# Performance work log

Hardware: AMD Instinct MI355X
Metric: run time of the kernel (lower is better)

Reference implementation:

```python
import jax, jax.numpy as jnp
import numpy as np

STU_N, EXER_N, K_N, EMB = 20000, 20000, 128, 128
BATCH = 4096

def _pos(w):
    # PosLinear weight transform: 2*relu(-w) + w  (== |w|)
    return 2.0 * jax.nn.relu(-w) + w

def setup_inputs() -> dict:
    key = jax.random.key(0)
    ks = jax.random.split(key, 12)
    xav = lambda k, shape: jax.random.normal(k, shape, jnp.float32) * np.sqrt(2.0 / sum(shape))
    return {
        "stu_id": jax.random.randint(ks[0], (BATCH,), 0, STU_N, jnp.int32),
        "exer_id": jax.random.randint(ks[1], (BATCH,), 0, EXER_N, jnp.int32),
        "kq": jax.random.uniform(ks[2], (BATCH, K_N), jnp.float32),
        "student_q": xav(ks[3], (STU_N, EMB)),
        "exercise_k": xav(ks[4], (EXER_N, EMB)),
        "student_v": xav(ks[5], (STU_N, EMB)),
        "exercise_v": xav(ks[6], (EXER_N, EMB)),
        "knowledge_v": xav(ks[7], (K_N, EMB)),
        "W1": xav(ks[8], (EMB, 2 * EMB)), "b1": jnp.zeros((EMB,), jnp.float32),
        "W2": xav(ks[9], (EMB, 2 * EMB)), "b2": jnp.zeros((EMB,), jnp.float32),
        "W3": xav(ks[10], (1, EMB)), "b3": jnp.zeros((1,), jnp.float32),
    }

def reference(stu_id, exer_id, kq, student_q, exercise_k, student_v, exercise_v,
              knowledge_v, W1, b1, W2, b2, W3, b3):
    stu_q = student_q[stu_id]          # (B, D)
    exer_k = exercise_k[exer_id]       # (B, D)
    stu_v = student_v[stu_id]          # (B, D)
    exer_v = exercise_v[exer_id]       # (B, D)
    B, D = stu_v.shape
    K = knowledge_v.shape[0]

    kn = jnp.broadcast_to(knowledge_v[None, :, :], (B, K, D))
    stu_b = jnp.broadcast_to(stu_v[:, None, :], (B, K, D))
    exer_b = jnp.broadcast_to(exer_v[:, None, :], (B, K, D))

    # PosLinear 1/2 on concat([x, kn]) -> split GEMM avoids materializing concat
    W1p, W2p, W3p = _pos(W1), _pos(W2), _pos(W3)
    pref = jax.nn.sigmoid(jnp.einsum('bkd,ed->bke', jnp.concatenate([stu_b, kn], -1), W1p) + b1)
    diff = jax.nn.sigmoid(jnp.einsum('bkd,ed->bke', jnp.concatenate([exer_b, kn], -1), W2p) + b2)

    disc = jax.nn.sigmoid(stu_q * exer_k)              # (B, D)
    input_x = (pref - diff) * disc[:, None, :]         # (B, K, D)
    o = jax.nn.sigmoid(jnp.einsum('bkd,od->bko', input_x, W3p) + b3)  # (B, K, 1)

    sum_out = jnp.sum(o * kq[:, :, None], axis=1)      # (B, 1)
    count = jnp.sum(kq, axis=1, keepdims=True)         # (B, 1)
    return jnp.squeeze(sum_out / count)                # (B,)
```

## Files before the change

### kernel.cpp

```cpp
#include <hip/hip_runtime.h>

#define D  128
#define KN 128
#define NB 16
#define LOG2E 1.44269504088896340736f

typedef float f32x4  __attribute__((ext_vector_type(4)));
typedef float f32x16 __attribute__((ext_vector_type(16)));
typedef short s16x8  __attribute__((ext_vector_type(8)));

__device__ __forceinline__ float negexp(float v) {
    return __builtin_amdgcn_exp2f(v * -LOG2E);
}
__device__ __forceinline__ float sigf(float x) {
    return __builtin_amdgcn_rcpf(1.0f + negexp(x));
}
__device__ __forceinline__ unsigned short f2bf(float f) {
    unsigned u = __float_as_uint(f);
    return (unsigned short)((u + 0x7fffu + ((u >> 16) & 1u)) >> 16);
}
__device__ __forceinline__ s16x8 pack8(float4 a, float4 b) {
    s16x8 r;
    r[0]=(short)f2bf(a.x); r[1]=(short)f2bf(a.y); r[2]=(short)f2bf(a.z); r[3]=(short)f2bf(a.w);
    r[4]=(short)f2bf(b.x); r[5]=(short)f2bf(b.y); r[6]=(short)f2bf(b.z); r[7]=(short)f2bf(b.w);
    return r;
}
__device__ __forceinline__ s16x8 pack8abs(float4 a, float4 b) {
    s16x8 r;
    r[0]=(short)f2bf(fabsf(a.x)); r[1]=(short)f2bf(fabsf(a.y)); r[2]=(short)f2bf(fabsf(a.z)); r[3]=(short)f2bf(fabsf(a.w));
    r[4]=(short)f2bf(fabsf(b.x)); r[5]=(short)f2bf(fabsf(b.y)); r[6]=(short)f2bf(fabsf(b.z)); r[7]=(short)f2bf(fabsf(b.w));
    return r;
}

#define CORE(EA1, EA2, T, PZ, A0, A1) do {                                   \
    float x0_ = fmaf((EA1), (T).x, 1.0f);                                    \
    float x1_ = fmaf((EA1), (T).y, 1.0f);                                    \
    float y0_ = fmaf((EA2), (T).z, 1.0f);                                    \
    float y1_ = fmaf((EA2), (T).w, 1.0f);                                    \
    (A0) = fmaf((y0_ - x0_) * (PZ), __builtin_amdgcn_rcpf(x0_ * y0_), (A0)); \
    (A1) = fmaf((y1_ - x1_) * (PZ), __builtin_amdgcn_rcpf(x1_ * y1_), (A1)); \
} while (0)

#define TTILE(T, ACC) {                                                       \
    const int idx_ = (wid << 2) + (T);                                        \
    const char* Wsb_ = (idx_ < 16) ? W1s_base : W2s_base;                     \
    const int et_ = (idx_ >> 2) & 3, kt_ = idx_ & 3;                          \
    const int er_ = et_ * 32 + l31, kr_ = kt_ * 32 + l31;                     \
    const int eswz_ = (er_ & 7) << 4, kswz_ = (kr_ & 7) << 4;                 \
    _Pragma("unroll")                                                         \
    for (int q = 0; q < 8; ++q) {                                             \
        int dby = q * 32 + g32 * 16;                                          \
        s16x8 a_ = *(const s16x8*)(Wsb_ + er_ * 256 + (dby ^ eswz_));         \
        s16x8 b_ = *(const s16x8*)(KNs_base + kr_ * 256 + (dby ^ kswz_));     \
        ACC = __builtin_amdgcn_mfma_f32_32x32x16_bf16(a_, b_, ACC, 0, 0, 0);  \
    } }

#define TWRITE(T, ACC) {                                                      \
    const int idx_ = (wid << 2) + (T);                                        \
    const int et_ = (idx_ >> 2) & 3, kt_ = idx_ & 3;                          \
    const int slot_ = (idx_ < 16) ? 0 : 2;                                    \
    const float* bias_ = (idx_ < 16) ? b1 : b2;                               \
    const int k_ = kt_ * 32 + l31;                                            \
    const int kof_ = ((k_ >> 1) << 2) + (k_ & 1) + slot_;                     \
    _Pragma("unroll")                                                         \
    for (int r = 0; r < 16; ++r) {                                            \
        int e_ = et_ * 32 + (r & 3) + ((r >> 2) << 3) + (g32 << 2);           \
        TABf[e_ * 256 + kof_] = negexp(ACC[r] + bias_[e_]);                   \
    } }

__global__ __launch_bounds__(512, 1) void fused_kernel(
    const int* __restrict__ stu_id, const int* __restrict__ exer_id,
    const float* __restrict__ kq,
    const float* __restrict__ stu_q, const float* __restrict__ exer_k,
    const float* __restrict__ stu_v, const float* __restrict__ exer_v,
    const float* __restrict__ kn,
    const float* __restrict__ W1, const float* __restrict__ b1,
    const float* __restrict__ W2, const float* __restrict__ b2,
    const float* __restrict__ W3, const float* __restrict__ b3,
    float* __restrict__ out, int B)
{
    __shared__ float4 smem4[9728];
    __shared__ int sids[NB], eids[NB];

    float* TABf = (float*)smem4;
    float* EAf  = TABf + 32768;
    float* PZf  = EAf + 4096;
    char* KNs_base = (char*)smem4;
    char* W1s_base = KNs_base + 32768;
    char* W2s_base = KNs_base + 65536;

    const int tid  = threadIdx.x;
    const int b0   = blockIdx.x * NB;
    const int lane = tid & 63, wid = tid >> 6;
    const int l31 = lane & 31, g32 = lane >> 5;
    const int l15 = lane & 15, g16 = lane >> 4;

    if (tid < NB) {
        int b = b0 + tid;
        sids[tid] = stu_id[b < B ? b : 0];
        eids[tid] = exer_id[b < B ? b : 0];
    }
    for (int i = tid; i < 128 * 16; i += 512) {
        int row = i >> 4, c = i & 15;
        int byt = row * 256 + (((c << 4)) ^ ((row & 7) << 4));
        const float4* sk = (const float4*)(kn + (size_t)row * D + c * 8);
        *(s16x8*)(KNs_base + byt) = pack8(sk[0], sk[1]);
        const float4* s1 = (const float4*)(W1 + (size_t)row * (2 * D) + D + c * 8);
        *(s16x8*)(W1s_base + byt) = pack8abs(s1[0], s1[1]);
        const float4* s2 = (const float4*)(W2 + (size_t)row * (2 * D) + D + c * 8);
        *(s16x8*)(W2s_base + byt) = pack8abs(s2[0], s2[1]);
    }
    __syncthreads();

    f32x16 t0acc = {0}, t1acc = {0}, t2acc = {0}, t3acc = {0};
    TTILE(0, t0acc) TTILE(1, t1acc) TTILE(2, t2acc) TTILE(3, t3acc)

    const int sid_l = sids[l15], eid_l = eids[l15];
    const int erow  = wid * 16 + l15;
    f32x4 accS = {0, 0, 0, 0}, accE = {0, 0, 0, 0};
    #pragma unroll
    for (int q = 0; q < 4; ++q) {
        int d = q * 32 + g16 * 8;
        const float4* pa = (const float4*)(stu_v + (size_t)sid_l * D + d);
        const float4* pb = (const float4*)(W1 + (size_t)erow * (2 * D) + d);
        accS = __builtin_amdgcn_mfma_f32_16x16x32_bf16(
            pack8(pa[0], pa[1]), pack8abs(pb[0], pb[1]), accS, 0, 0, 0);
        const float4* pe = (const float4*)(exer_v + (size_t)eid_l * D + d);
        const float4* pc = (const float4*)(W2 + (size_t)erow * (2 * D) + d);
        accE = __builtin_amdgcn_mfma_f32_16x16x32_bf16(
            pack8(pe[0], pe[1]), pack8abs(pc[0], pc[1]), accE, 0, 0, 0);
    }
    #pragma unroll
    for (int r = 0; r < 4; ++r) {
        int b = g16 * 4 + r;
        int eo = b * 256 + 2 * erow;
        EAf[eo]     = negexp(accS[r]);
        EAf[eo + 1] = negexp(accE[r]);
    }
    {
        int b = tid >> 5, e4 = (tid & 31) << 2;
        float4 sq = *(const float4*)(stu_q + (size_t)sids[b] * D + e4);
        float4 ek = *(const float4*)(exer_k + (size_t)eids[b] * D + e4);
        float4 w3 = *(const float4*)(W3 + e4);
        float4 z;
        z.x = sigf(sq.x * ek.x) * fabsf(w3.x);
        z.y = sigf(sq.y * ek.y) * fabsf(w3.y);
        z.z = sigf(sq.z * ek.z) * fabsf(w3.z);
        z.w = sigf(sq.w * ek.w) * fabsf(w3.w);
        *(float4*)(PZf + b * D + e4) = z;
    }
    __syncthreads();

    TWRITE(0, t0acc) TWRITE(1, t1acc) TWRITE(2, t2acc) TWRITE(3, t3acc)
    __syncthreads();

    const float4* TAB4 = (const float4*)TABf;
    const float4* EA4  = (const float4*)EAf;
    const float2* PZ2  = (const float2*)PZf;
    const float b3v = b3[0];
    const int rA = 2 * wid, rB = 2 * wid + 1;
    const int bA = b0 + rA, bB = b0 + rB;

    float acc0a = 0.f, acc1a = 0.f, acc0b = 0.f, acc1b = 0.f;
    #pragma unroll 2
    for (int j = 0; j < D / 2; ++j) {
        float4 t0 = TAB4[(2 * j) * 64 + lane];
        float4 t1 = TAB4[(2 * j + 1) * 64 + lane];
        float4 eA = EA4[rA * 64 + j]; float2 zA = PZ2[rA * 64 + j];
        float4 eB = EA4[rB * 64 + j]; float2 zB = PZ2[rB * 64 + j];
        CORE(eA.x, eA.y, t0, zA.x, acc0a, acc1a);
        CORE(eA.z, eA.w, t1, zA.y, acc0a, acc1a);
        CORE(eB.x, eB.y, t0, zB.x, acc0b, acc1b);
        CORE(eB.z, eB.w, t1, zB.y, acc0b, acc1b);
    }

    float o0a = sigf(acc0a + b3v), o1a = sigf(acc1a + b3v);
    float o0b = sigf(acc0b + b3v), o1b = sigf(acc1b + b3v);
    float na = 0.f, da = 0.f, nb = 0.f, db = 0.f;
    if (bA < B) {
        float2 kqa = *(const float2*)(kq + (size_t)bA * D + 2 * lane);
        na = fmaf(o0a, kqa.x, o1a * kqa.y); da = kqa.x + kqa.y;
    }
    if (bB < B) {
        float2 kqb = *(const float2*)(kq + (size_t)bB * D + 2 * lane);
        nb = fmaf(o0b, kqb.x, o1b * kqb.y); db = kqb.x + kqb.y;
    }
    #pragma unroll
    for (int off = 32; off > 0; off >>= 1) {
        na += __shfl_xor(na, off); da += __shfl_xor(da, off);
        nb += __shfl_xor(nb, off); db += __shfl_xor(db, off);
    }
    if (lane == 0) {
        if (bA < B) out[bA] = na / da;
        if (bB < B) out[bB] = nb / db;
    }
}

extern "C" void kernel_launch(void* const* d_in, const int* in_sizes, int n_in,
                              void* d_out, int out_size, void* d_ws, size_t ws_size,
                              hipStream_t stream)
{
    const int*   stu_id      = (const int*)  d_in[0];
    const int*   exer_id     = (const int*)  d_in[1];
    const float* kq          = (const float*)d_in[2];
    const float* student_q   = (const float*)d_in[3];
    const float* exercise_k  = (const float*)d_in[4];
    const float* student_v   = (const float*)d_in[5];
    const float* exercise_v  = (const float*)d_in[6];
    const float* knowledge_v = (const float*)d_in[7];
    const float* W1 = (const float*)d_in[8];
    const float* b1 = (const float*)d_in[9];
    const float* W2 = (const float*)d_in[10];
    const float* b2 = (const float*)d_in[11];
    const float* W3 = (const float*)d_in[12];
    const float* b3 = (const float*)d_in[13];
    float* out = (float*)d_out;
    const int B = in_sizes[0];

    int nblk = (B + NB - 1) / NB;
    fused_kernel<<<nblk, 512, 0, stream>>>(
        stu_id, exer_id, kq, student_q, exercise_k, student_v, exercise_v,
        knowledge_v, W1, b1, W2, b2, W3, b3, out, B);
}
```

Before: 32.41 us.

## Split main loop over embedding dim across waves, reuse A fragments, reduce via LDS

The table GEMM now has each wave own one 32-row E tile of W1 or W2 and compute all four K tiles. This loads the A fragment once per step and reuses it across four MFMAs. The gathered stu_v/exer_v rows are prefetched into registers before the MFMA phase so global latency overlaps with it. The per-element core loop is re-partitioned so each wave handles 16 embedding columns for all 16 batch rows and reads each TAB row once instead of every wave reading all of them. Partial sums then go through an LDS reduction across waves, at the cost of an extra barrier pair, extra LDS traffic and more registers (16 float2 accumulators plus 16 float4 prefetch registers).

```diff
diff --git a/kernel.cpp b/kernel.cpp
--- a/kernel.cpp
+++ b/kernel.cpp
@@ -40,20 +40,6 @@
     (A0) = fmaf((y0_ - x0_) * (PZ), __builtin_amdgcn_rcpf(x0_ * y0_), (A0)); \
     (A1) = fmaf((y1_ - x1_) * (PZ), __builtin_amdgcn_rcpf(x1_ * y1_), (A1)); \
 } while (0)
-
-#define TTILE(T, ACC) {                                                       \
-    const int idx_ = (wid << 2) + (T);                                        \
-    const char* Wsb_ = (idx_ < 16) ? W1s_base : W2s_base;                     \
-    const int et_ = (idx_ >> 2) & 3, kt_ = idx_ & 3;                          \
-    const int er_ = et_ * 32 + l31, kr_ = kt_ * 32 + l31;                     \
-    const int eswz_ = (er_ & 7) << 4, kswz_ = (kr_ & 7) << 4;                 \
-    _Pragma("unroll")                                                         \
-    for (int q = 0; q < 8; ++q) {                                             \
-        int dby = q * 32 + g32 * 16;                                          \
-        s16x8 a_ = *(const s16x8*)(Wsb_ + er_ * 256 + (dby ^ eswz_));         \
-        s16x8 b_ = *(const s16x8*)(KNs_base + kr_ * 256 + (dby ^ kswz_));     \
-        ACC = __builtin_amdgcn_mfma_f32_32x32x16_bf16(a_, b_, ACC, 0, 0, 0);  \
-    } }
 
 #define TWRITE(T, ACC) {                                                      \
     const int idx_ = (wid << 2) + (T);                                        \
@@ -112,23 +98,49 @@
     }
     __syncthreads();
 
-    f32x16 t0acc = {0}, t1acc = {0}, t2acc = {0}, t3acc = {0};
-    TTILE(0, t0acc) TTILE(1, t1acc) TTILE(2, t2acc) TTILE(3, t3acc)
-
     const int sid_l = sids[l15], eid_l = eids[l15];
     const int erow  = wid * 16 + l15;
-    f32x4 accS = {0, 0, 0, 0}, accE = {0, 0, 0, 0};
+    float4 ga[8], ge[8];
     #pragma unroll
     for (int q = 0; q < 4; ++q) {
         int d = q * 32 + g16 * 8;
         const float4* pa = (const float4*)(stu_v + (size_t)sid_l * D + d);
+        ga[2*q] = pa[0]; ga[2*q+1] = pa[1];
+        const float4* pe = (const float4*)(exer_v + (size_t)eid_l * D + d);
+        ge[2*q] = pe[0]; ge[2*q+1] = pe[1];
+    }
+
+    f32x16 t0acc = {0}, t1acc = {0}, t2acc = {0}, t3acc = {0};
+    {
+        const char* Wsb = (wid < 4) ? W1s_base : W2s_base;
+        const int er = (wid & 3) * 32 + l31;
+        const int eswz = (er & 7) << 4;
+        const int kswz = (l31 & 7) << 4;
+        #pragma unroll
+        for (int q = 0; q < 8; ++q) {
+            int dby = q * 32 + g32 * 16;
+            s16x8 a_  = *(const s16x8*)(Wsb + er * 256 + (dby ^ eswz));
+            s16x8 bb0 = *(const s16x8*)(KNs_base + (  0 + l31) * 256 + (dby ^ kswz));
+            s16x8 bb1 = *(const s16x8*)(KNs_base + ( 32 + l31) * 256 + (dby ^ kswz));
+            s16x8 bb2 = *(const s16x8*)(KNs_base + ( 64 + l31) * 256 + (dby ^ kswz));
+            s16x8 bb3 = *(const s16x8*)(KNs_base + ( 96 + l31) * 256 + (dby ^ kswz));
+            t0acc = __builtin_amdgcn_mfma_f32_32x32x16_bf16(a_, bb0, t0acc, 0, 0, 0);
+            t1acc = __builtin_amdgcn_mfma_f32_32x32x16_bf16(a_, bb1, t1acc, 0, 0, 0);
+            t2acc = __builtin_amdgcn_mfma_f32_32x32x16_bf16(a_, bb2, t2acc, 0, 0, 0);
+            t3acc = __builtin_amdgcn_mfma_f32_32x32x16_bf16(a_, bb3, t3acc, 0, 0, 0);
+        }
+    }
+
+    f32x4 accS = {0, 0, 0, 0}, accE = {0, 0, 0, 0};
+    #pragma unroll
+    for (int q = 0; q < 4; ++q) {
+        int d = q * 32 + g16 * 8;
         const float4* pb = (const float4*)(W1 + (size_t)erow * (2 * D) + d);
         accS = __builtin_amdgcn_mfma_f32_16x16x32_bf16(
-            pack8(pa[0], pa[1]), pack8abs(pb[0], pb[1]), accS, 0, 0, 0);
-        const float4* pe = (const float4*)(exer_v + (size_t)eid_l * D + d);
+            pack8(ga[2*q], ga[2*q+1]), pack8abs(pb[0], pb[1]), accS, 0, 0, 0);
         const float4* pc = (const float4*)(W2 + (size_t)erow * (2 * D) + d);
         accE = __builtin_amdgcn_mfma_f32_16x16x32_bf16(
-            pack8(pe[0], pe[1]), pack8abs(pc[0], pc[1]), accE, 0, 0, 0);
+            pack8(ge[2*q], ge[2*q+1]), pack8abs(pc[0], pc[1]), accE, 0, 0, 0);
     }
     #pragma unroll
     for (int r = 0; r < 4; ++r) {
@@ -157,25 +169,47 @@
     const float4* TAB4 = (const float4*)TABf;
     const float4* EA4  = (const float4*)EAf;
     const float2* PZ2  = (const float2*)PZf;
+
+    float2 acc[16];
+    #pragma unroll
+    for (int r = 0; r < 16; ++r) acc[r] = make_float2(0.f, 0.f);
+
+    for (int jj = 0; jj < 8; ++jj) {
+        const int e0 = wid * 16 + 2 * jj;
+        const int jg = wid * 8 + jj;
+        float4 t0 = TAB4[e0 * 64 + lane];
+        float4 t1 = TAB4[(e0 + 1) * 64 + lane];
+        #pragma unroll
+        for (int r = 0; r < 16; ++r) {
+            float4 eA = EA4[r * 64 + jg];
+            float2 zA = PZ2[r * 64 + jg];
+            CORE(eA.x, eA.y, t0, zA.x, acc[r].x, acc[r].y);
+            CORE(eA.z, eA.w, t1, zA.y, acc[r].x, acc[r].y);
+        }
+    }
+    __syncthreads();
+
+    float2* RED = (float2*)TABf;
+    #pragma unroll
+    for (int r = 0; r < 16; ++r)
+        RED[(wid * 16 + r) * 64 + lane] = acc[r];
+    __syncthreads();
+
     const float b3v = b3[0];
     const int rA = 2 * wid, rB = 2 * wid + 1;
     const int bA = b0 + rA, bB = b0 + rB;
 
-    float acc0a = 0.f, acc1a = 0.f, acc0b = 0.f, acc1b = 0.f;
-    #pragma unroll 2
-    for (int j = 0; j < D / 2; ++j) {
-        float4 t0 = TAB4[(2 * j) * 64 + lane];
-        float4 t1 = TAB4[(2 * j + 1) * 64 + lane];
-        float4 eA = EA4[rA * 64 + j]; float2 zA = PZ2[rA * 64 + j];
-        float4 eB = EA4[rB * 64 + j]; float2 zB = PZ2[rB * 64 + j];
-        CORE(eA.x, eA.y, t0, zA.x, acc0a, acc1a);
-        CORE(eA.z, eA.w, t1, zA.y, acc0a, acc1a);
-        CORE(eB.x, eB.y, t0, zB.x, acc0b, acc1b);
-        CORE(eB.z, eB.w, t1, zB.y, acc0b, acc1b);
-    }
-
-    float o0a = sigf(acc0a + b3v), o1a = sigf(acc1a + b3v);
-    float o0b = sigf(acc0b + b3v), o1b = sigf(acc1b + b3v);
+    float2 sA = make_float2(0.f, 0.f), sB = make_float2(0.f, 0.f);
+    #pragma unroll
+    for (int w = 0; w < 8; ++w) {
+        float2 pA = RED[(w * 16 + rA) * 64 + lane];
+        float2 pB = RED[(w * 16 + rB) * 64 + lane];
+        sA.x += pA.x; sA.y += pA.y;
+        sB.x += pB.x; sB.y += pB.y;
+    }
+
+    float o0a = sigf(sA.x + b3v), o1a = sigf(sA.y + b3v);
+    float o0b = sigf(sB.x + b3v), o1b = sigf(sB.y + b3v);
     float na = 0.f, da = 0.f, nb = 0.f, db = 0.f;
     if (bA < B) {
         float2 kqa = *(const float2*)(kq + (size_t)bA * D + 2 * lane);
```

Measured after the change: 31.43 us. 1.03x faster.
